# Performance work log

Hardware: AMD Instinct MI355X
Metric: run time of the kernel (lower is better)

Reference implementation:

```python
import jax, jax.numpy as jnp
import numpy as np
from jax import lax

B, S, M, D, H, T = 8, 128, 128, 256, 256, 256  # M == S required by reshape_adj; D == H required by tag FFNs and edge h0


def setup_inputs() -> dict:
    key = jax.random.key(0)
    ks = jax.random.split(key, 26)
    w = lambda k, shape: (jax.random.normal(k, shape, jnp.float32) * 0.05)
    lengths = jax.random.randint(ks[0], (B,), S // 2, S + 1)
    mask = (jnp.arange(S)[None, :] < lengths[:, None]).astype(jnp.int32)
    return {
        "input": jax.random.normal(ks[1], (B, S, D), jnp.float32),
        "tag_embeddings": jax.random.normal(ks[2], (B, S, 128), jnp.float32),
        "mask": mask,
        "head_indices": jax.random.randint(ks[3], (B, S), 0, S),
        "head_tags": jax.random.randint(ks[4], (B, S), 0, 40),
        # graph_rnn (2-layer tanh RNN, input D -> hidden H)
        "gW_ih0": w(ks[5], (H, D)), "gW_hh0": w(ks[6], (H, H)),
        "gb_ih0": w(ks[7], (H,)), "gb_hh0": w(ks[8], (H,)),
        "gW_ih1": w(ks[9], (H, H)), "gW_hh1": w(ks[10], (H, H)),
        "gb_ih1": w(ks[11], (H,)), "gb_hh1": w(ks[12], (H,)),
        # edge_rnn (2-layer tanh RNN, input M -> hidden H)
        "eW_ih0": w(ks[13], (H, M)), "eW_hh0": w(ks[14], (H, H)),
        "eb_ih0": w(ks[15], (H,)), "eb_hh0": w(ks[16], (H,)),
        "eW_ih1": w(ks[17], (H, H)), "eW_hh1": w(ks[18], (H, H)),
        "eb_ih1": w(ks[19], (H,)), "eb_hh1": w(ks[20], (H,)),
        # edge classifier + tag feedforwards
        "cls_W": w(ks[21], (1, H)), "cls_b": w(ks[22], (1,)),
        "head_W": w(ks[23], (T, H)), "head_b": jnp.zeros((T,), jnp.float32),
        "dep_W": w(ks[24], (T, H)), "dep_b": jnp.zeros((T,), jnp.float32),
    }


def _forward(input, gW_ih0, gW_hh0, gb_ih0, gb_hh0, gW_ih1, gW_hh1, gb_ih1, gb_hh1,
             eW_ih0, eW_hh0, eb_ih0, eb_hh0, eW_ih1, eW_hh1, eb_ih1, eb_hh1,
             cls_W, cls_b, head_W, head_b, dep_W, dep_b, mask):
    Bv, Sv, Dv = input.shape
    lengths = mask.sum(axis=-1)                      # [B]
    valid = jnp.arange(Sv)[:, None] < lengths[None, :]  # [S,B] packed-sequence validity

    # ---- graph_pass: 2-layer tanh RNN over time, emulating pack/pad (frozen state + zero output on pads)
    xt = input.transpose(1, 0, 2)  # [S,B,D]

    def gstep(h, inp):
        x_t, v = inp
        v = v[:, None]
        h0 = jnp.tanh(x_t @ gW_ih0.T + gb_ih0 + h[0] @ gW_hh0.T + gb_hh0)
        h0 = jnp.where(v, h0, h[0])
        h1 = jnp.tanh(h0 @ gW_ih1.T + gb_ih1 + h[1] @ gW_hh1.T + gb_hh1)
        h1 = jnp.where(v, h1, h[1])
        y = jnp.where(v, h1, 0.0)
        return jnp.stack([h0, h1]), y

    hg0 = jnp.zeros((2, Bv, H), input.dtype)
    _, ys = lax.scan(gstep, hg0, (xt, valid))
    graph_states = ys.transpose(1, 0, 2)  # [B,S,H]

    # ---- edge_pass: sequential over M steps; positions i are independent -> fold S into batch
    gs = graph_states.reshape(Bv * Sv, H)
    hE0 = jnp.stack([gs, gs])              # (edge_l=2, B*S, H)
    A0 = jnp.zeros((Bv * Sv, M), input.dtype)

    def estep(carry, j):
        A_row, h = carry
        x = A_row  # input at every step is the current (partially filled) row, per the original
        e0 = jnp.tanh(x @ eW_ih0.T + eb_ih0 + h[0] @ eW_hh0.T + eb_hh0)
        e1 = jnp.tanh(e0 @ eW_ih1.T + eb_ih1 + h[1] @ eW_hh1.T + eb_hh1)
        edge = jax.nn.sigmoid(e1 @ cls_W.T + cls_b)[:, 0]  # [B*S]
        A_row = A_row.at[:, j].set(edge)
        return (A_row, jnp.stack([e0, e1])), None

    (A_flat, _), _ = lax.scan(estep, (A0, hE0), jnp.arange(M))
    A = A_flat.reshape(Bv, Sv, M)

    # ---- reshape_adj: with M == S, shift is always 0 -> strictly-lower-triangular mask, then transpose
    tri = jnp.tril(jnp.ones((Sv, M), bool), -1)
    arc_logits = jnp.where(tri[None, :, :], A, 0.0).transpose(0, 2, 1)

    # ---- tag feedforwards (dropout = identity in eval mode)
    head_tag = jax.nn.elu(graph_states @ head_W.T + head_b)
    dep_tag = jax.nn.elu(graph_states @ dep_W.T + dep_b)
    return head_tag, dep_tag, arc_logits


def reference(input, tag_embeddings, mask, head_indices, head_tags,
              gW_ih0, gW_hh0, gb_ih0, gb_hh0, gW_ih1, gW_hh1, gb_ih1, gb_hh1,
              eW_ih0, eW_hh0, eb_ih0, eb_hh0, eW_ih1, eW_hh1, eb_ih1, eb_hh1,
              cls_W, cls_b, head_W, head_b, dep_W, dep_b):
    # tag_embeddings, head_indices, head_tags are passed through unchanged in the original
    return _forward(input, gW_ih0, gW_hh0, gb_ih0, gb_hh0, gW_ih1, gW_hh1, gb_ih1, gb_hh1,
                    eW_ih0, eW_hh0, eb_ih0, eb_hh0, eW_ih1, eW_hh1, eb_ih1, eb_hh1,
                    cls_W, cls_b, head_W, head_b, dep_W, dep_b, mask)
```

## Files before the change

kernel.cpp:

```cpp
#include <hip/hip_runtime.h>
#include <hip/hip_bf16.h>

#define HH 256
#define SS 128
#define BB 8
#define MM 128
#define DD 256
#define TT 256
#define GG 16
#define NW 8

#define ROWG 33
#define FBE (16 * ROWG * 8)
#define FB1 (ROWG * 8)

typedef float  f32x4  __attribute__((ext_vector_type(4)));
typedef short  bf16x8 __attribute__((ext_vector_type(8)));

__device__ __forceinline__ float bflo(unsigned int u) { return __uint_as_float(u << 16); }
__device__ __forceinline__ float bfhi(unsigned int u) { return __uint_as_float(u & 0xffff0000u); }
__device__ __forceinline__ float bfs(unsigned short s) { return __uint_as_float(((unsigned)s) << 16); }
__device__ __forceinline__ unsigned short f2bf(float x) {
    unsigned u = __float_as_uint(x);
    return (unsigned short)((u + 0x7fffu + ((u >> 16) & 1u)) >> 16);
}
__device__ __forceinline__ unsigned pk2bf(float a, float b) {
    return (unsigned)f2bf(a) | ((unsigned)f2bf(b) << 16);
}
__device__ __forceinline__ float ftanh(float x) {
    float e = __expf(2.0f * x);
    return 1.0f - 2.0f * __builtin_amdgcn_rcpf(e + 1.0f);
}
__device__ __forceinline__ float fsigm(float x) {
    return __builtin_amdgcn_rcpf(1.0f + __expf(-x));
}

__global__ void k_prep(const float* __restrict__ gW_hh0, const float* __restrict__ gW_ih1,
                       const float* __restrict__ gW_hh1, const float* __restrict__ eW_hh0,
                       const float* __restrict__ eW_ih1, const float* __restrict__ eW_hh1,
                       const float* __restrict__ head_W, const float* __restrict__ dep_W,
                       const float* __restrict__ eW_ih0,
                       unsigned short* __restrict__ pk_g0, unsigned short* __restrict__ pk_g1,
                       unsigned short* __restrict__ pk_g2, unsigned short* __restrict__ pk_e0,
                       unsigned short* __restrict__ pk_e1, unsigned short* __restrict__ pk_e2,
                       unsigned short* __restrict__ pk_h0, unsigned short* __restrict__ pk_h1,
                       unsigned short* __restrict__ eWTb) {
    int m = blockIdx.x >> 5;
    int blk = blockIdx.x & 31;
    if (m < 8) {
        const float* W = (m == 0) ? gW_hh0 : (m == 1) ? gW_ih1 : (m == 2) ? gW_hh1
                       : (m == 3) ? eW_hh0 : (m == 4) ? eW_ih1 : (m == 5) ? eW_hh1
                       : (m == 6) ? head_W : dep_W;
        unsigned short* pk = (m == 0) ? pk_g0 : (m == 1) ? pk_g1 : (m == 2) ? pk_g2
                           : (m == 3) ? pk_e0 : (m == 4) ? pk_e1 : (m == 5) ? pk_e2
                           : (m == 6) ? pk_h0 : pk_h1;
        int idx = blk * 256 + threadIdx.x;
        int f = idx >> 6, l = idx & 63;
        int ct = f >> 3, kb = f & 7, q = l >> 4, mm = l & 15;
        unsigned short out[8];
#pragma unroll
        for (int e = 0; e < 8; e++) {
            int k = kb * 32 + q * 4 + (e & 3) + ((e >> 2) << 4);
            out[e] = f2bf(W[(ct * 16 + mm) * HH + k]);
        }
        uint4 v;
        v.x = out[0] | ((unsigned)out[1] << 16);
        v.y = out[2] | ((unsigned)out[3] << 16);
        v.z = out[4] | ((unsigned)out[5] << 16);
        v.w = out[6] | ((unsigned)out[7] << 16);
        *(uint4*)(pk + idx * 8) = v;
    } else {
        int base = blk * 256 + threadIdx.x;
#pragma unroll
        for (int k = 0; k < 4; k++) {
            int idx = base + k * 8192;
            int j = idx >> 8, c = idx & 255;
            eWTb[idx] = f2bf(eW_ih0[c * MM + j]);
        }
    }
}

__global__ void k_x0(const float* __restrict__ x, const float* __restrict__ Wih0,
                     const float* __restrict__ bih0, const float* __restrict__ bhh0,
                     unsigned short* __restrict__ X0B) {
    int row = blockIdx.x;
    int i = threadIdx.x;
    const float4* xr = (const float4*)(x + row * DD);
    const float4* wr = (const float4*)(Wih0 + i * DD);
    float a0 = 0.f, a1 = 0.f, a2 = 0.f, a3 = 0.f;
#pragma unroll 8
    for (int k = 0; k < DD / 4; k++) {
        float4 xv = xr[k]; float4 wv = wr[k];
        a0 += xv.x * wv.x; a1 += xv.y * wv.y; a2 += xv.z * wv.z; a3 += xv.w * wv.w;
    }
    X0B[row * HH + i] = f2bf(a0 + a1 + a2 + a3 + bih0[i] + bhh0[i]);
}

__device__ __forceinline__ bf16x8 ldA(const unsigned short* __restrict__ pk, int ct, int kb, int lane) {
    return *(const bf16x8*)(pk + (((ct * 8 + kb) * 64 + lane) << 3));
}
__device__ __forceinline__ bf16x8 ldBf(const unsigned short* base, int row, int kb, int q) {
    return *(const bf16x8*)(base + ((row * ROWG + kb * 4 + q) << 3));
}

__global__ __launch_bounds__(512, 2) void k_graph_mfma(
    const unsigned short* __restrict__ X0B, const int* __restrict__ mask,
    const unsigned short* __restrict__ pk0,
    const unsigned short* __restrict__ pk1,
    const unsigned short* __restrict__ pk2,
    const float* __restrict__ bih1, const float* __restrict__ bhh1,
    float* __restrict__ GS) {
    __shared__ alignas(16) unsigned short xs[SS * HH];
    __shared__ alignas(16) unsigned short gs[SS * HH];
    __shared__ alignas(16) unsigned short h0b[2 * FB1];
    __shared__ alignas(16) unsigned short h1b[3 * FB1];
    __shared__ int lenS;

    int b = blockIdx.x;
    int tid = threadIdx.x;
    int wv = tid >> 6, lane = tid & 63;
    int q = lane >> 4, rr = lane & 15;
    int ct0 = 2 * wv;
    int m0 = 32 * wv + 4 * q;
    int g16off = (wv * 4 + q) << 3;

    { unsigned* p = (unsigned*)h0b; for (int i = tid; i < FB1; i += 512) p[i] = 0; }
    { unsigned* p = (unsigned*)h1b; for (int i = tid; i < 3 * FB1 / 2; i += 512) p[i] = 0; }
    {
        const uint4* s = (const uint4*)(X0B + b * SS * HH);
        uint4* d = (uint4*)xs;
        for (int i = tid; i < SS * HH / 8; i += 512) d[i] = s[i];
    }
    if (wv == 0) {
        int s = mask[b * SS + lane] + mask[b * SS + 64 + lane];
        for (int off = 32; off; off >>= 1) s += __shfl_xor(s, off);
        if (lane == 0) lenS = s;
    }
    bf16x8 a0[2][8], a1[2][8], a2[2][8];
#pragma unroll
    for (int kb = 0; kb < 8; kb++) {
        a0[0][kb] = ldA(pk0, ct0, kb, lane); a0[1][kb] = ldA(pk0, ct0 + 1, kb, lane);
        a1[0][kb] = ldA(pk1, ct0, kb, lane); a1[1][kb] = ldA(pk1, ct0 + 1, kb, lane);
        a2[0][kb] = ldA(pk2, ct0, kb, lane); a2[1][kb] = ldA(pk2, ct0 + 1, kb, lane);
    }
#pragma unroll
    for (int kb = 0; kb < 8; kb++) {
        asm volatile("" : "+v"(a0[0][kb]), "+v"(a0[1][kb]),
                          "+v"(a1[0][kb]), "+v"(a1[1][kb]),
                          "+v"(a2[0][kb]), "+v"(a2[1][kb]));
    }
    f32x4 b1A = *(const f32x4*)(bih1 + m0) + *(const f32x4*)(bhh1 + m0);
    f32x4 b1B = *(const f32x4*)(bih1 + m0 + 16) + *(const f32x4*)(bhh1 + m0 + 16);
    __syncthreads();
    int len = lenS;
    bool w0l = (rr == 0);

    {
        ushort4 xa = *(const ushort4*)(xs + m0);
        ushort4 xb = *(const ushort4*)(xs + m0 + 16);
        if (w0l) {
            uint4 nv = { pk2bf(ftanh(bfs(xa.x)), ftanh(bfs(xa.y))),
                         pk2bf(ftanh(bfs(xa.z)), ftanh(bfs(xa.w))),
                         pk2bf(ftanh(bfs(xb.x)), ftanh(bfs(xb.y))),
                         pk2bf(ftanh(bfs(xb.z)), ftanh(bfs(xb.w))) };
            *(uint4*)(h0b + g16off) = nv;
        }
    }
    __syncthreads();

    int ir = 2, iw = 0;
    for (int t = 1; t < len; t++) {
        const unsigned short* h0r = h0b + ((t - 1) & 1) * FB1;
        const unsigned short* h1r = h1b + ir * FB1;
        ushort4 xa = *(const ushort4*)(xs + t * 256 + m0);
        ushort4 xb = *(const ushort4*)(xs + t * 256 + m0 + 16);
        f32x4 accA0 = { bfs(xa.x), bfs(xa.y), bfs(xa.z), bfs(xa.w) };
        f32x4 accB0 = { bfs(xb.x), bfs(xb.y), bfs(xb.z), bfs(xb.w) };
        f32x4 accA1 = {0.f,0.f,0.f,0.f}, accB1 = {0.f,0.f,0.f,0.f};
        f32x4 pAe = b1A, pBe = b1B;
        f32x4 pAh = {0.f,0.f,0.f,0.f}, pBh = {0.f,0.f,0.f,0.f};
#pragma unroll
        for (int kb = 0; kb < 4; kb++) {
            bf16x8 h = ldBf(h0r, 0, kb, q);
            bf16x8 g = ldBf(h1r, 0, kb, q);
            accA0 = __builtin_amdgcn_mfma_f32_16x16x32_bf16(a0[0][kb], h, accA0, 0, 0, 0);
            accB0 = __builtin_amdgcn_mfma_f32_16x16x32_bf16(a0[1][kb], h, accB0, 0, 0, 0);
            pAe   = __builtin_amdgcn_mfma_f32_16x16x32_bf16(a1[0][kb], h, pAe, 0, 0, 0);
            pBe   = __builtin_amdgcn_mfma_f32_16x16x32_bf16(a1[1][kb], h, pBe, 0, 0, 0);
            pAh   = __builtin_amdgcn_mfma_f32_16x16x32_bf16(a2[0][kb], g, pAh, 0, 0, 0);
            pBh   = __builtin_amdgcn_mfma_f32_16x16x32_bf16(a2[1][kb], g, pBh, 0, 0, 0);
        }
#pragma unroll
        for (int kb = 4; kb < 8; kb++) {
            bf16x8 h = ldBf(h0r, 0, kb, q);
            bf16x8 g = ldBf(h1r, 0, kb, q);
            accA1 = __builtin_amdgcn_mfma_f32_16x16x32_bf16(a0[0][kb], h, accA1, 0, 0, 0);
            accB1 = __builtin_amdgcn_mfma_f32_16x16x32_bf16(a0[1][kb], h, accB1, 0, 0, 0);
            pAe   = __builtin_amdgcn_mfma_f32_16x16x32_bf16(a1[0][kb], h, pAe, 0, 0, 0);
            pBe   = __builtin_amdgcn_mfma_f32_16x16x32_bf16(a1[1][kb], h, pBe, 0, 0, 0);
            pAh   = __builtin_amdgcn_mfma_f32_16x16x32_bf16(a2[0][kb], g, pAh, 0, 0, 0);
            pBh   = __builtin_amdgcn_mfma_f32_16x16x32_bf16(a2[1][kb], g, pBh, 0, 0, 0);
        }
        if (w0l) {
            f32x4 accA = accA0 + accA1, accB = accB0 + accB1;
            uint4 nv0 = { pk2bf(ftanh(accA[0]), ftanh(accA[1])), pk2bf(ftanh(accA[2]), ftanh(accA[3])),
                          pk2bf(ftanh(accB[0]), ftanh(accB[1])), pk2bf(ftanh(accB[2]), ftanh(accB[3])) };
            *(uint4*)(h0b + (t & 1) * FB1 + g16off) = nv0;
            f32x4 pA = pAe + pAh, pB = pBe + pBh;
            float eA[4], eB[4];
#pragma unroll
            for (int r = 0; r < 4; r++) { eA[r] = ftanh(pA[r]); eB[r] = ftanh(pB[r]); }
            uint4 nv1 = { pk2bf(eA[0], eA[1]), pk2bf(eA[2], eA[3]),
                          pk2bf(eB[0], eB[1]), pk2bf(eB[2], eB[3]) };
            *(uint4*)(h1b + iw * FB1 + g16off) = nv1;
            ushort4 ga = { f2bf(eA[0]), f2bf(eA[1]), f2bf(eA[2]), f2bf(eA[3]) };
            ushort4 gb = { f2bf(eB[0]), f2bf(eB[1]), f2bf(eB[2]), f2bf(eB[3]) };
            *(ushort4*)(gs + (t - 1) * 256 + m0) = ga;
            *(ushort4*)(gs + (t - 1) * 256 + m0 + 16) = gb;
        }
        __syncthreads();
        ir = (ir + 1 == 3) ? 0 : ir + 1;
        iw = (iw + 1 == 3) ? 0 : iw + 1;
    }

    {
        const unsigned short* h0r = h0b + ((len - 1) & 1) * FB1;
        const unsigned short* h1r = h1b + ir * FB1;
        f32x4 pAe = b1A, pBe = b1B;
        f32x4 pAh = {0.f,0.f,0.f,0.f}, pBh = {0.f,0.f,0.f,0.f};
#pragma unroll
        for (int kb = 0; kb < 8; kb++) {
            bf16x8 h = ldBf(h0r, 0, kb, q);
            bf16x8 g = ldBf(h1r, 0, kb, q);
            pAe = __builtin_amdgcn_mfma_f32_16x16x32_bf16(a1[0][kb], h, pAe, 0, 0, 0);
            pBe = __builtin_amdgcn_mfma_f32_16x16x32_bf16(a1[1][kb], h, pBe, 0, 0, 0);
            pAh = __builtin_amdgcn_mfma_f32_16x16x32_bf16(a2[0][kb], g, pAh, 0, 0, 0);
            pBh = __builtin_amdgcn_mfma_f32_16x16x32_bf16(a2[1][kb], g, pBh, 0, 0, 0);
        }
        if (w0l) {
            f32x4 pA = pAe + pAh, pB = pBe + pBh;
            ushort4 ga = { f2bf(ftanh(pA[0])), f2bf(ftanh(pA[1])), f2bf(ftanh(pA[2])), f2bf(ftanh(pA[3])) };
            ushort4 gb = { f2bf(ftanh(pB[0])), f2bf(ftanh(pB[1])), f2bf(ftanh(pB[2])), f2bf(ftanh(pB[3])) };
            *(ushort4*)(gs + (len - 1) * 256 + m0) = ga;
            *(ushort4*)(gs + (len - 1) * 256 + m0 + 16) = gb;
        }
    }
    __syncthreads();
    {
        float* dst = GS + b * (SS * HH);
        const uint4* src = (const uint4*)gs;
        for (int i = tid; i < SS * HH / 8; i += 512) {
            int t = i >> 5;
            float4 f0 = {0.f,0.f,0.f,0.f}, f1 = {0.f,0.f,0.f,0.f};
            if (t < len) {
                uint4 v = src[i];
                f0 = float4{ bflo(v.x), bfhi(v.x), bflo(v.y), bfhi(v.y) };
                f1 = float4{ bflo(v.z), bfhi(v.z), bflo(v.w), bfhi(v.w) };
            }
            *(float4*)(dst + i * 8) = f0;
            *(float4*)(dst + i * 8 + 4) = f1;
        }
    }
}

__global__ __launch_bounds__(512, 2) void k_edge_mfma(
    const float* __restrict__ GS,
    const unsigned short* __restrict__ pk0,
    const unsigned short* __restrict__ pk1,
    const unsigned short* __restrict__ pk2,
    const unsigned short* __restrict__ pkh,
    const unsigned short* __restrict__ pkd,
    const unsigned short* __restrict__ eWTb,
    const float* __restrict__ bih0, const float* __restrict__ bhh0,
    const float* __restrict__ bih1, const float* __restrict__ bhh1,
    const float* __restrict__ clsW, const float* __restrict__ clsB,
    const float* __restrict__ headB, const float* __restrict__ depB,
    float* __restrict__ arc, float* __restrict__ headO, float* __restrict__ depO) {
    __shared__ alignas(16) unsigned short h0f[2 * FBE];
    __shared__ alignas(16) unsigned short h1f[2 * FBE];
    __shared__ alignas(16) unsigned short gsf[FBE];
    __shared__ alignas(16) unsigned short ews[MM * HH];
    __shared__ float red[NW][GG];
    __shared__ float cws[HH];
    __shared__ float b1s[HH];
    __shared__ float arcb[GG][MM + 1];

    int tid = threadIdx.x;
    int wv = tid >> 6, lane = tid & 63;
    int q = lane >> 4, rr = lane & 15;
    int m0 = 32 * wv + 4 * q;
    int goff = (rr * ROWG + wv * 4 + q) << 3;
    int r0 = blockIdx.x * GG;

    {
        const uint4* s = (const uint4*)eWTb;
        uint4* d = (uint4*)ews;
        for (int i = tid; i < MM * HH / 8; i += 512) d[i] = s[i];
    }
    {
        int r = tid >> 5, g = tid & 31;
        int kb = g >> 2, qq = g & 3;
        int lo = kb * 32 + qq * 4;
        const float* gp = GS + (r0 + r) * HH + lo;
        float4 vlo = *(const float4*)gp;
        float4 vhi = *(const float4*)(gp + 16);
        uint4 pv = { pk2bf(vlo.x, vlo.y), pk2bf(vlo.z, vlo.w),
                     pk2bf(vhi.x, vhi.y), pk2bf(vhi.z, vhi.w) };
        int off = (r * ROWG + g) << 3;
        *(uint4*)(h0f + FBE + off) = pv;
        *(uint4*)(h1f + FBE + off) = pv;
        *(uint4*)(gsf + off) = pv;
        *(uint4*)(h1f + off) = uint4{0,0,0,0};
        *(uint4*)(h0f + off) = uint4{0,0,0,0};
    }
    if (tid < HH) {
        cws[tid] = clsW[tid];
        b1s[tid] = bih1[tid] + bhh1[tid];
    }
    bf16x8 a0[2][8], a1[2][8], a2[2][8];
#pragma unroll
    for (int kb = 0; kb < 8; kb++) {
        a0[0][kb] = ldA(pk0, 2 * wv, kb, lane); a0[1][kb] = ldA(pk0, 2 * wv + 1, kb, lane);
        a1[0][kb] = ldA(pk1, 2 * wv, kb, lane); a1[1][kb] = ldA(pk1, 2 * wv + 1, kb, lane);
        a2[0][kb] = ldA(pk2, 2 * wv, kb, lane); a2[1][kb] = ldA(pk2, 2 * wv + 1, kb, lane);
    }
#pragma unroll
    for (int kb = 0; kb < 8; kb++) {
        asm volatile("" : "+v"(a0[0][kb]), "+v"(a0[1][kb]),
                          "+v"(a1[0][kb]), "+v"(a1[1][kb]),
                          "+v"(a2[0][kb]), "+v"(a2[1][kb]));
    }
    f32x4 xw0A = *(const f32x4*)(bih0 + m0) + *(const f32x4*)(bhh0 + m0);
    f32x4 xw0B = *(const f32x4*)(bih0 + m0 + 16) + *(const f32x4*)(bhh0 + m0 + 16);
    float clsb = clsB[0];
    int srow = (r0 + tid) & 127;
    __syncthreads();

    for (int j = 0; j <= MM; j++) {
        const unsigned short* h0r = h0f + ((j + 1) & 1) * FBE;
        const unsigned short* h1r = h1f + (j & 1) * FBE;
        f32x4 acc0 = xw0A, acc1 = xw0B;
        f32x4 p0e = *(const f32x4*)&b1s[m0];
        f32x4 p1e = *(const f32x4*)&b1s[m0 + 16];
        f32x4 p0h = {0.f,0.f,0.f,0.f}, p1h = {0.f,0.f,0.f,0.f};
#pragma unroll
        for (int kb = 0; kb < 8; kb++) {
            bf16x8 b0 = ldBf(h0r, rr, kb, q);
            bf16x8 b1 = ldBf(h1r, rr, kb, q);
            acc0 = __builtin_amdgcn_mfma_f32_16x16x32_bf16(a0[0][kb], b0, acc0, 0, 0, 0);
            acc1 = __builtin_amdgcn_mfma_f32_16x16x32_bf16(a0[1][kb], b0, acc1, 0, 0, 0);
            p0e  = __builtin_amdgcn_mfma_f32_16x16x32_bf16(a1[0][kb], b0, p0e, 0, 0, 0);
            p1e  = __builtin_amdgcn_mfma_f32_16x16x32_bf16(a1[1][kb], b0, p1e, 0, 0, 0);
            p0h  = __builtin_amdgcn_mfma_f32_16x16x32_bf16(a2[0][kb], b1, p0h, 0, 0, 0);
            p1h  = __builtin_amdgcn_mfma_f32_16x16x32_bf16(a2[1][kb], b1, p1h, 0, 0, 0);
        }
        if (j > 0) {
            float e1a[4], e1b[4];
#pragma unroll
            for (int r = 0; r < 4; r++) { e1a[r] = ftanh(p0e[r] + p0h[r]); e1b[r] = ftanh(p1e[r] + p1h[r]); }
            uint4 nv = { pk2bf(e1a[0], e1a[1]), pk2bf(e1a[2], e1a[3]),
                         pk2bf(e1b[0], e1b[1]), pk2bf(e1b[2], e1b[3]) };
            *(uint4*)(h1f + ((j + 1) & 1) * FBE + goff) = nv;
            f32x4 cwA = *(const f32x4*)&cws[m0];
            f32x4 cwB = *(const f32x4*)&cws[m0 + 16];
            float part = cwA[0] * e1a[0] + cwA[1] * e1a[1] + cwA[2] * e1a[2] + cwA[3] * e1a[3]
                       + cwB[0] * e1b[0] + cwB[1] * e1b[1] + cwB[2] * e1b[2] + cwB[3] * e1b[3];
            part += __shfl_xor(part, 16);
            part += __shfl_xor(part, 32);
            if (lane < 16) red[wv][lane] = part;
        }
        __syncthreads();
        if (j > 0) {
            float s = clsb;
#pragma unroll
            for (int w = 0; w < NW; w++) s += red[w][rr];
            float edge = fsigm(s);
            ushort4 ewcA = *(const ushort4*)(ews + (j - 1) * HH + m0);
            ushort4 ewcB = *(const ushort4*)(ews + (j - 1) * HH + m0 + 16);
            f32x4 ewA = { bfs(ewcA.x), bfs(ewcA.y), bfs(ewcA.z), bfs(ewcA.w) };
            f32x4 ewB = { bfs(ewcB.x), bfs(ewcB.y), bfs(ewcB.z), bfs(ewcB.w) };
            xw0A += edge * ewA;  acc0 += edge * ewA;
            xw0B += edge * ewB;  acc1 += edge * ewB;
            if (tid < GG) arcb[tid][j - 1] = ((j - 1) < srow) ? edge : 0.f;
        }
        if (j < MM) {
            uint4 nv = { pk2bf(ftanh(acc0[0]), ftanh(acc0[1])), pk2bf(ftanh(acc0[2]), ftanh(acc0[3])),
                         pk2bf(ftanh(acc1[0]), ftanh(acc1[1])), pk2bf(ftanh(acc1[2]), ftanh(acc1[3])) };
            *(uint4*)(h0f + (j & 1) * FBE + goff) = nv;
        }
        __syncthreads();
    }
    for (int i = tid; i < GG * MM; i += 512) {
        int row = i & 15, j = i >> 4;
        int sr = (r0 + row) & 127, bi = (r0 + row) >> 7;
        arc[bi * (MM * SS) + j * SS + sr] = arcb[row][j];
    }
    {
        f32x4 hA = *(const f32x4*)(headB + m0);
        f32x4 hB = *(const f32x4*)(headB + m0 + 16);
        f32x4 dA = *(const f32x4*)(depB + m0);
        f32x4 dB = *(const f32x4*)(depB + m0 + 16);
#pragma unroll
        for (int kb = 0; kb < 8; kb++) {
            bf16x8 bg = ldBf(gsf, rr, kb, q);
            hA = __builtin_amdgcn_mfma_f32_16x16x32_bf16(ldA(pkh, 2 * wv, kb, lane), bg, hA, 0, 0, 0);
            hB = __builtin_amdgcn_mfma_f32_16x16x32_bf16(ldA(pkh, 2 * wv + 1, kb, lane), bg, hB, 0, 0, 0);
            dA = __builtin_amdgcn_mfma_f32_16x16x32_bf16(ldA(pkd, 2 * wv, kb, lane), bg, dA, 0, 0, 0);
            dB = __builtin_amdgcn_mfma_f32_16x16x32_bf16(ldA(pkd, 2 * wv + 1, kb, lane), bg, dB, 0, 0, 0);
        }
        int row = r0 + rr;
        f32x4 oA, oB, eA, eB;
#pragma unroll
        for (int r = 0; r < 4; r++) {
            oA[r] = (hA[r] > 0.f) ? hA[r] : (__expf(hA[r]) - 1.0f);
            oB[r] = (hB[r] > 0.f) ? hB[r] : (__expf(hB[r]) - 1.0f);
            eA[r] = (dA[r] > 0.f) ? dA[r] : (__expf(dA[r]) - 1.0f);
            eB[r] = (dB[r] > 0.f) ? dB[r] : (__expf(dB[r]) - 1.0f);
        }
        *(f32x4*)(headO + row * TT + m0) = oA;
        *(f32x4*)(headO + row * TT + m0 + 16) = oB;
        *(f32x4*)(depO + row * TT + m0) = eA;
        *(f32x4*)(depO + row * TT + m0 + 16) = eB;
    }
}

extern "C" void kernel_launch(void* const* d_in, const int* in_sizes, int n_in,
                              void* d_out, int out_size, void* d_ws, size_t ws_size,
                              hipStream_t stream) {
    const float* input  = (const float*)d_in[0];
    const int*   mask   = (const int*)d_in[2];
    const float* gW_ih0 = (const float*)d_in[5];
    const float* gW_hh0 = (const float*)d_in[6];
    const float* gb_ih0 = (const float*)d_in[7];
    const float* gb_hh0 = (const float*)d_in[8];
    const float* gW_ih1 = (const float*)d_in[9];
    const float* gW_hh1 = (const float*)d_in[10];
    const float* gb_ih1 = (const float*)d_in[11];
    const float* gb_hh1 = (const float*)d_in[12];
    const float* eW_ih0 = (const float*)d_in[13];
    const float* eW_hh0 = (const float*)d_in[14];
    const float* eb_ih0 = (const float*)d_in[15];
    const float* eb_hh0 = (const float*)d_in[16];
    const float* eW_ih1 = (const float*)d_in[17];
    const float* eW_hh1 = (const float*)d_in[18];
    const float* eb_ih1 = (const float*)d_in[19];
    const float* eb_hh1 = (const float*)d_in[20];
    const float* cls_W  = (const float*)d_in[21];
    const float* cls_b  = (const float*)d_in[22];
    const float* head_W = (const float*)d_in[23];
    const float* head_b = (const float*)d_in[24];
    const float* dep_W  = (const float*)d_in[25];
    const float* dep_b  = (const float*)d_in[26];

    float* out      = (float*)d_out;
    float* head_out = out;
    float* dep_out  = out + 262144;
    float* arc_out  = out + 524288;

    char* ws = (char*)d_ws;
    unsigned short* X0B = (unsigned short*)ws;
    float* GS  = (float*)(ws + (1 << 20));
    unsigned short* pk_g0 = (unsigned short*)(ws + (2 << 20));
    unsigned short* pk_g1 = pk_g0 + 65536;
    unsigned short* pk_g2 = pk_g0 + 2 * 65536;
    unsigned short* pk_e0 = pk_g0 + 3 * 65536;
    unsigned short* pk_e1 = pk_g0 + 4 * 65536;
    unsigned short* pk_e2 = pk_g0 + 5 * 65536;
    unsigned short* pk_h0 = pk_g0 + 6 * 65536;
    unsigned short* pk_h1 = pk_g0 + 7 * 65536;
    unsigned short* eWTb  = pk_g0 + 8 * 65536;

    k_prep<<<288, 256, 0, stream>>>(gW_hh0, gW_ih1, gW_hh1, eW_hh0, eW_ih1, eW_hh1,
                                    head_W, dep_W, eW_ih0,
                                    pk_g0, pk_g1, pk_g2, pk_e0, pk_e1, pk_e2,
                                    pk_h0, pk_h1, eWTb);
    k_x0<<<1024, 256, 0, stream>>>(input, gW_ih0, gb_ih0, gb_hh0, X0B);
    k_graph_mfma<<<8, 512, 0, stream>>>(X0B, mask, pk_g0, pk_g1, pk_g2, gb_ih1, gb_hh1, GS);
    k_edge_mfma<<<64, 512, 0, stream>>>(GS, pk_e0, pk_e1, pk_e2, pk_h0, pk_h1, eWTb,
                                        eb_ih0, eb_hh0, eb_ih1, eb_hh1, cls_W, cls_b,
                                        head_b, dep_b, arc_out, head_out, dep_out);
}
```

Before: 487.3 us.

## Restructure edge RNN to four waves with in-step layer-1 dependency chain

```diff
diff --git a/kernel.cpp b/kernel.cpp
--- a/kernel.cpp
+++ b/kernel.cpp
@@ -9,6 +9,7 @@
 #define TT 256
 #define GG 16
 #define NW 8
+#define NWE 4
 
 #define ROWG 33
 #define FBE (16 * ROWG * 8)
@@ -263,7 +264,7 @@
     }
 }
 
-__global__ __launch_bounds__(512, 2) void k_edge_mfma(
+__global__ __launch_bounds__(256, 1) void k_edge_mfma(
     const float* __restrict__ GS,
     const unsigned short* __restrict__ pk0,
     const unsigned short* __restrict__ pk1,
@@ -280,7 +281,7 @@
     __shared__ alignas(16) unsigned short h1f[2 * FBE];
     __shared__ alignas(16) unsigned short gsf[FBE];
     __shared__ alignas(16) unsigned short ews[MM * HH];
-    __shared__ float red[NW][GG];
+    __shared__ float red[NWE][GG];
     __shared__ float cws[HH];
     __shared__ float b1s[HH];
     __shared__ float arcb[GG][MM + 1];
@@ -288,17 +289,19 @@
     int tid = threadIdx.x;
     int wv = tid >> 6, lane = tid & 63;
     int q = lane >> 4, rr = lane & 15;
-    int m0 = 32 * wv + 4 * q;
-    int goff = (rr * ROWG + wv * 4 + q) << 3;
     int r0 = blockIdx.x * GG;
+    int mb = 64 * wv + 4 * q;
+    int goffA = (rr * ROWG + 8 * wv + q) << 3;
+    int goffB = (rr * ROWG + 8 * wv + 4 + q) << 3;
 
     {
         const uint4* s = (const uint4*)eWTb;
         uint4* d = (uint4*)ews;
-        for (int i = tid; i < MM * HH / 8; i += 512) d[i] = s[i];
-    }
-    {
-        int r = tid >> 5, g = tid & 31;
+        for (int i = tid; i < MM * HH / 8; i += 256) d[i] = s[i];
+    }
+#pragma unroll
+    for (int rb = 0; rb < 16; rb += 8) {
+        int r = (tid >> 5) + rb, g = tid & 31;
         int kb = g >> 2, qq = g & 3;
         int lo = kb * 32 + qq * 4;
         const float* gp = GS + (r0 + r) * HH + lo;
@@ -307,120 +310,143 @@
         uint4 pv = { pk2bf(vlo.x, vlo.y), pk2bf(vlo.z, vlo.w),
                      pk2bf(vhi.x, vhi.y), pk2bf(vhi.z, vhi.w) };
         int off = (r * ROWG + g) << 3;
-        *(uint4*)(h0f + FBE + off) = pv;
-        *(uint4*)(h1f + FBE + off) = pv;
+        *(uint4*)(h0f + off) = pv;
+        *(uint4*)(h1f + off) = pv;
         *(uint4*)(gsf + off) = pv;
-        *(uint4*)(h1f + off) = uint4{0,0,0,0};
-        *(uint4*)(h0f + off) = uint4{0,0,0,0};
-    }
-    if (tid < HH) {
-        cws[tid] = clsW[tid];
-        b1s[tid] = bih1[tid] + bhh1[tid];
-    }
-    bf16x8 a0[2][8], a1[2][8], a2[2][8];
+    }
+    cws[tid] = clsW[tid];
+    b1s[tid] = bih1[tid] + bhh1[tid];
+    bf16x8 a0[4][8], a1[4][8], a2[4][8];
 #pragma unroll
     for (int kb = 0; kb < 8; kb++) {
-        a0[0][kb] = ldA(pk0, 2 * wv, kb, lane); a0[1][kb] = ldA(pk0, 2 * wv + 1, kb, lane);
-        a1[0][kb] = ldA(pk1, 2 * wv, kb, lane); a1[1][kb] = ldA(pk1, 2 * wv + 1, kb, lane);
-        a2[0][kb] = ldA(pk2, 2 * wv, kb, lane); a2[1][kb] = ldA(pk2, 2 * wv + 1, kb, lane);
+#pragma unroll
+        for (int c = 0; c < 4; c++) {
+            a0[c][kb] = ldA(pk0, 4 * wv + c, kb, lane);
+            a1[c][kb] = ldA(pk1, 4 * wv + c, kb, lane);
+            a2[c][kb] = ldA(pk2, 4 * wv + c, kb, lane);
+        }
     }
 #pragma unroll
     for (int kb = 0; kb < 8; kb++) {
-        asm volatile("" : "+v"(a0[0][kb]), "+v"(a0[1][kb]),
-                          "+v"(a1[0][kb]), "+v"(a1[1][kb]),
-                          "+v"(a2[0][kb]), "+v"(a2[1][kb]));
-    }
-    f32x4 xw0A = *(const f32x4*)(bih0 + m0) + *(const f32x4*)(bhh0 + m0);
-    f32x4 xw0B = *(const f32x4*)(bih0 + m0 + 16) + *(const f32x4*)(bhh0 + m0 + 16);
+        asm volatile("" : "+v"(a0[0][kb]), "+v"(a0[1][kb]), "+v"(a0[2][kb]), "+v"(a0[3][kb]),
+                          "+v"(a1[0][kb]), "+v"(a1[1][kb]), "+v"(a1[2][kb]), "+v"(a1[3][kb]),
+                          "+v"(a2[0][kb]), "+v"(a2[1][kb]), "+v"(a2[2][kb]), "+v"(a2[3][kb]));
+    }
+    f32x4 xw0[4];
+#pragma unroll
+    for (int c = 0; c < 4; c++) {
+        xw0[c] = *(const f32x4*)(bih0 + mb + 16 * c) + *(const f32x4*)(bhh0 + mb + 16 * c);
+    }
     float clsb = clsB[0];
     int srow = (r0 + tid) & 127;
     __syncthreads();
 
-    for (int j = 0; j <= MM; j++) {
-        const unsigned short* h0r = h0f + ((j + 1) & 1) * FBE;
-        const unsigned short* h1r = h1f + (j & 1) * FBE;
-        f32x4 acc0 = xw0A, acc1 = xw0B;
-        f32x4 p0e = *(const f32x4*)&b1s[m0];
-        f32x4 p1e = *(const f32x4*)&b1s[m0 + 16];
-        f32x4 p0h = {0.f,0.f,0.f,0.f}, p1h = {0.f,0.f,0.f,0.f};
+    for (int j = 0; j < MM; j++) {
+        int jr = j & 1, jw = jr ^ 1;
+        const unsigned short* rb0 = h0f + jr * FBE;
+        f32x4 acc[4];
+#pragma unroll
+        for (int c = 0; c < 4; c++) acc[c] = xw0[c];
 #pragma unroll
         for (int kb = 0; kb < 8; kb++) {
-            bf16x8 b0 = ldBf(h0r, rr, kb, q);
-            bf16x8 b1 = ldBf(h1r, rr, kb, q);
-            acc0 = __builtin_amdgcn_mfma_f32_16x16x32_bf16(a0[0][kb], b0, acc0, 0, 0, 0);
-            acc1 = __builtin_amdgcn_mfma_f32_16x16x32_bf16(a0[1][kb], b0, acc1, 0, 0, 0);
-            p0e  = __builtin_amdgcn_mfma_f32_16x16x32_bf16(a1[0][kb], b0, p0e, 0, 0, 0);
-            p1e  = __builtin_amdgcn_mfma_f32_16x16x32_bf16(a1[1][kb], b0, p1e, 0, 0, 0);
-            p0h  = __builtin_amdgcn_mfma_f32_16x16x32_bf16(a2[0][kb], b1, p0h, 0, 0, 0);
-            p1h  = __builtin_amdgcn_mfma_f32_16x16x32_bf16(a2[1][kb], b1, p1h, 0, 0, 0);
-        }
-        if (j > 0) {
-            float e1a[4], e1b[4];
-#pragma unroll
-            for (int r = 0; r < 4; r++) { e1a[r] = ftanh(p0e[r] + p0h[r]); e1b[r] = ftanh(p1e[r] + p1h[r]); }
-            uint4 nv = { pk2bf(e1a[0], e1a[1]), pk2bf(e1a[2], e1a[3]),
-                         pk2bf(e1b[0], e1b[1]), pk2bf(e1b[2], e1b[3]) };
-            *(uint4*)(h1f + ((j + 1) & 1) * FBE + goff) = nv;
-            f32x4 cwA = *(const f32x4*)&cws[m0];
-            f32x4 cwB = *(const f32x4*)&cws[m0 + 16];
-            float part = cwA[0] * e1a[0] + cwA[1] * e1a[1] + cwA[2] * e1a[2] + cwA[3] * e1a[3]
-                       + cwB[0] * e1b[0] + cwB[1] * e1b[1] + cwB[2] * e1b[2] + cwB[3] * e1b[3];
-            part += __shfl_xor(part, 16);
-            part += __shfl_xor(part, 32);
-            if (lane < 16) red[wv][lane] = part;
+            bf16x8 b0 = ldBf(rb0, rr, kb, q);
+#pragma unroll
+            for (int c = 0; c < 4; c++)
+                acc[c] = __builtin_amdgcn_mfma_f32_16x16x32_bf16(a0[c][kb], b0, acc[c], 0, 0, 0);
+        }
+        {
+            uint4 nvA = { pk2bf(ftanh(acc[0][0]), ftanh(acc[0][1])), pk2bf(ftanh(acc[0][2]), ftanh(acc[0][3])),
+                          pk2bf(ftanh(acc[1][0]), ftanh(acc[1][1])), pk2bf(ftanh(acc[1][2]), ftanh(acc[1][3])) };
+            uint4 nvB = { pk2bf(ftanh(acc[2][0]), ftanh(acc[2][1])), pk2bf(ftanh(acc[2][2]), ftanh(acc[2][3])),
+                          pk2bf(ftanh(acc[3][0]), ftanh(acc[3][1])), pk2bf(ftanh(acc[3][2]), ftanh(acc[3][3])) };
+            *(uint4*)(h0f + jw * FBE + goffA) = nvA;
+            *(uint4*)(h0f + jw * FBE + goffB) = nvB;
         }
         __syncthreads();
-        if (j > 0) {
-            float s = clsb;
-#pragma unroll
-            for (int w = 0; w < NW; w++) s += red[w][rr];
-            float edge = fsigm(s);
-            ushort4 ewcA = *(const ushort4*)(ews + (j - 1) * HH + m0);
-            ushort4 ewcB = *(const ushort4*)(ews + (j - 1) * HH + m0 + 16);
-            f32x4 ewA = { bfs(ewcA.x), bfs(ewcA.y), bfs(ewcA.z), bfs(ewcA.w) };
-            f32x4 ewB = { bfs(ewcB.x), bfs(ewcB.y), bfs(ewcB.z), bfs(ewcB.w) };
-            xw0A += edge * ewA;  acc0 += edge * ewA;
-            xw0B += edge * ewB;  acc1 += edge * ewB;
-            if (tid < GG) arcb[tid][j - 1] = ((j - 1) < srow) ? edge : 0.f;
-        }
-        if (j < MM) {
-            uint4 nv = { pk2bf(ftanh(acc0[0]), ftanh(acc0[1])), pk2bf(ftanh(acc0[2]), ftanh(acc0[3])),
-                         pk2bf(ftanh(acc1[0]), ftanh(acc1[1])), pk2bf(ftanh(acc1[2]), ftanh(acc1[3])) };
-            *(uint4*)(h0f + (j & 1) * FBE + goff) = nv;
-        }
+        const unsigned short* rn = h0f + jw * FBE;
+        const unsigned short* r1 = h1f + jr * FBE;
+        f32x4 p[4];
+#pragma unroll
+        for (int c = 0; c < 4; c++) p[c] = *(const f32x4*)&b1s[mb + 16 * c];
+#pragma unroll
+        for (int kb = 0; kb < 8; kb++) {
+            bf16x8 be = ldBf(rn, rr, kb, q);
+            bf16x8 bh = ldBf(r1, rr, kb, q);
+#pragma unroll
+            for (int c = 0; c < 4; c++) {
+                p[c] = __builtin_amdgcn_mfma_f32_16x16x32_bf16(a1[c][kb], be, p[c], 0, 0, 0);
+                p[c] = __builtin_amdgcn_mfma_f32_16x16x32_bf16(a2[c][kb], bh, p[c], 0, 0, 0);
+            }
+        }
+        float e1[4][4];
+        float part = 0.f;
+#pragma unroll
+        for (int c = 0; c < 4; c++) {
+            f32x4 cw = *(const f32x4*)&cws[mb + 16 * c];
+#pragma unroll
+            for (int r = 0; r < 4; r++) {
+                e1[c][r] = ftanh(p[c][r]);
+                part += cw[r] * e1[c][r];
+            }
+        }
+        {
+            uint4 nvA = { pk2bf(e1[0][0], e1[0][1]), pk2bf(e1[0][2], e1[0][3]),
+                          pk2bf(e1[1][0], e1[1][1]), pk2bf(e1[1][2], e1[1][3]) };
+            uint4 nvB = { pk2bf(e1[2][0], e1[2][1]), pk2bf(e1[2][2], e1[2][3]),
+                          pk2bf(e1[3][0], e1[3][1]), pk2bf(e1[3][2], e1[3][3]) };
+            *(uint4*)(h1f + jw * FBE + goffA) = nvA;
+            *(uint4*)(h1f + jw * FBE + goffB) = nvB;
+        }
+        part += __shfl_xor(part, 16);
+        part += __shfl_xor(part, 32);
+        if (lane < 16) red[wv][lane] = part;
         __syncthreads();
-    }
-    for (int i = tid; i < GG * MM; i += 512) {
+        float s = clsb;
+#pragma unroll
+        for (int w = 0; w < NWE; w++) s += red[w][rr];
+        float edge = fsigm(s);
+#pragma unroll
+        for (int c = 0; c < 4; c++) {
+            ushort4 ew = *(const ushort4*)(ews + j * HH + mb + 16 * c);
+            f32x4 ewf = { bfs(ew.x), bfs(ew.y), bfs(ew.z), bfs(ew.w) };
+            xw0[c] += edge * ewf;
+        }
+        if (tid < GG) arcb[tid][j] = (j < srow) ? edge : 0.f;
+    }
+    __syncthreads();
+    for (int i = tid; i < GG * MM; i += 256) {
         int row = i & 15, j = i >> 4;
         int sr = (r0 + row) & 127, bi = (r0 + row) >> 7;
         arc[bi * (MM * SS) + j * SS + sr] = arcb[row][j];
     }
     {
-        f32x4 hA = *(const f32x4*)(headB + m0);
-        f32x4 hB = *(const f32x4*)(headB + m0 + 16);
-        f32x4 dA = *(const f32x4*)(depB + m0);
-        f32x4 dB = *(const f32x4*)(depB + m0 + 16);
+        f32x4 hc[4], dc[4];
+#pragma unroll
+        for (int c = 0; c < 4; c++) {
+            hc[c] = *(const f32x4*)(headB + mb + 16 * c);
+            dc[c] = *(const f32x4*)(depB + mb + 16 * c);
+        }
 #pragma unroll
         for (int kb = 0; kb < 8; kb++) {
             bf16x8 bg = ldBf(gsf, rr, kb, q);
-            hA = __builtin_amdgcn_mfma_f32_16x16x32_bf16(ldA(pkh, 2 * wv, kb, lane), bg, hA, 0, 0, 0);
-            hB = __builtin_amdgcn_mfma_f32_16x16x32_bf16(ldA(pkh, 2 * wv + 1, kb, lane), bg, hB, 0, 0, 0);
-            dA = __builtin_amdgcn_mfma_f32_16x16x32_bf16(ldA(pkd, 2 * wv, kb, lane), bg, dA, 0, 0, 0);
-            dB = __builtin_amdgcn_mfma_f32_16x16x32_bf16(ldA(pkd, 2 * wv + 1, kb, lane), bg, dB, 0, 0, 0);
+#pragma unroll
+            for (int c = 0; c < 4; c++) {
+                hc[c] = __builtin_amdgcn_mfma_f32_16x16x32_bf16(ldA(pkh, 4 * wv + c, kb, lane), bg, hc[c], 0, 0, 0);
+                dc[c] = __builtin_amdgcn_mfma_f32_16x16x32_bf16(ldA(pkd, 4 * wv + c, kb, lane), bg, dc[c], 0, 0, 0);
+            }
         }
         int row = r0 + rr;
-        f32x4 oA, oB, eA, eB;
-#pragma unroll
-        for (int r = 0; r < 4; r++) {
-            oA[r] = (hA[r] > 0.f) ? hA[r] : (__expf(hA[r]) - 1.0f);
-            oB[r] = (hB[r] > 0.f) ? hB[r] : (__expf(hB[r]) - 1.0f);
-            eA[r] = (dA[r] > 0.f) ? dA[r] : (__expf(dA[r]) - 1.0f);
-            eB[r] = (dB[r] > 0.f) ? dB[r] : (__expf(dB[r]) - 1.0f);
-        }
-        *(f32x4*)(headO + row * TT + m0) = oA;
-        *(f32x4*)(headO + row * TT + m0 + 16) = oB;
-        *(f32x4*)(depO + row * TT + m0) = eA;
-        *(f32x4*)(depO + row * TT + m0 + 16) = eB;
+#pragma unroll
+        for (int c = 0; c < 4; c++) {
+            f32x4 ho, dd;
+#pragma unroll
+            for (int r = 0; r < 4; r++) {
+                ho[r] = (hc[c][r] > 0.f) ? hc[c][r] : (__expf(hc[c][r]) - 1.0f);
+                dd[r] = (dc[c][r] > 0.f) ? dc[c][r] : (__expf(dc[c][r]) - 1.0f);
+            }
+            *(f32x4*)(headO + row * TT + mb + 16 * c) = ho;
+            *(f32x4*)(depO + row * TT + mb + 16 * c) = dd;
+        }
     }
 }
 
@@ -476,7 +502,7 @@
                                     pk_h0, pk_h1, eWTb);
     k_x0<<<1024, 256, 0, stream>>>(input, gW_ih0, gb_ih0, gb_hh0, X0B);
     k_graph_mfma<<<8, 512, 0, stream>>>(X0B, mask, pk_g0, pk_g1, pk_g2, gb_ih1, gb_hh1, GS);
-    k_edge_mfma<<<64, 512, 0, stream>>>(GS, pk_e0, pk_e1, pk_e2, pk_h0, pk_h1, eWTb,
+    k_edge_mfma<<<64, 256, 0, stream>>>(GS, pk_e0, pk_e1, pk_e2, pk_h0, pk_h1, eWTb,
                                         eb_ih0, eb_hh0, eb_ih1, eb_hh1, cls_W, cls_b,
                                         head_b, dep_b, arc_out, head_out, dep_out);
 }
```

After: 588.6 us. +20.8%, slower.

## Unskew edge RNN loop so each step runs layer 0 then layer 1

Applied to the files above, without the earlier changes.

```diff
diff --git a/kernel.cpp b/kernel.cpp
--- a/kernel.cpp
+++ b/kernel.cpp
@@ -276,8 +276,8 @@
     const float* __restrict__ clsW, const float* __restrict__ clsB,
     const float* __restrict__ headB, const float* __restrict__ depB,
     float* __restrict__ arc, float* __restrict__ headO, float* __restrict__ depO) {
-    __shared__ alignas(16) unsigned short h0f[2 * FBE];
-    __shared__ alignas(16) unsigned short h1f[2 * FBE];
+    __shared__ alignas(16) unsigned short h0[2 * FBE];
+    __shared__ alignas(16) unsigned short h1[2 * FBE];
     __shared__ alignas(16) unsigned short gsf[FBE];
     __shared__ alignas(16) unsigned short ews[MM * HH];
     __shared__ float red[NW][GG];
@@ -307,11 +307,9 @@
         uint4 pv = { pk2bf(vlo.x, vlo.y), pk2bf(vlo.z, vlo.w),
                      pk2bf(vhi.x, vhi.y), pk2bf(vhi.z, vhi.w) };
         int off = (r * ROWG + g) << 3;
-        *(uint4*)(h0f + FBE + off) = pv;
-        *(uint4*)(h1f + FBE + off) = pv;
+        *(uint4*)(h0 + off) = pv;
+        *(uint4*)(h1 + off) = pv;
         *(uint4*)(gsf + off) = pv;
-        *(uint4*)(h1f + off) = uint4{0,0,0,0};
-        *(uint4*)(h0f + off) = uint4{0,0,0,0};
     }
     if (tid < HH) {
         cws[tid] = clsW[tid];
@@ -336,60 +334,70 @@
     int srow = (r0 + tid) & 127;
     __syncthreads();
 
-    for (int j = 0; j <= MM; j++) {
-        const unsigned short* h0r = h0f + ((j + 1) & 1) * FBE;
-        const unsigned short* h1r = h1f + (j & 1) * FBE;
+    ushort4 ewcA = *(const ushort4*)(ews + m0);
+    ushort4 ewcB = *(const ushort4*)(ews + m0 + 16);
+
+    for (int j = 0; j < MM; j++) {
+        int jr = j & 1, jw = jr ^ 1;
+        const unsigned short* rb0 = h0 + jr * FBE;
         f32x4 acc0 = xw0A, acc1 = xw0B;
+#pragma unroll
+        for (int kb = 0; kb < 8; kb++) {
+            bf16x8 b = ldBf(rb0, rr, kb, q);
+            acc0 = __builtin_amdgcn_mfma_f32_16x16x32_bf16(a0[0][kb], b, acc0, 0, 0, 0);
+            acc1 = __builtin_amdgcn_mfma_f32_16x16x32_bf16(a0[1][kb], b, acc1, 0, 0, 0);
+        }
+        {
+            uint4 nv = { pk2bf(ftanh(acc0[0]), ftanh(acc0[1])), pk2bf(ftanh(acc0[2]), ftanh(acc0[3])),
+                         pk2bf(ftanh(acc1[0]), ftanh(acc1[1])), pk2bf(ftanh(acc1[2]), ftanh(acc1[3])) };
+            *(uint4*)(h0 + jw * FBE + goff) = nv;
+        }
+        __syncthreads();
+        int jn = (j + 1 < MM) ? j + 1 : j;
+        ushort4 ewnA = *(const ushort4*)(ews + jn * HH + m0);
+        ushort4 ewnB = *(const ushort4*)(ews + jn * HH + m0 + 16);
+        const unsigned short* rn = h0 + jw * FBE;
+        const unsigned short* r1 = h1 + jr * FBE;
         f32x4 p0e = *(const f32x4*)&b1s[m0];
         f32x4 p1e = *(const f32x4*)&b1s[m0 + 16];
         f32x4 p0h = {0.f,0.f,0.f,0.f}, p1h = {0.f,0.f,0.f,0.f};
 #pragma unroll
         for (int kb = 0; kb < 8; kb++) {
-            bf16x8 b0 = ldBf(h0r, rr, kb, q);
-            bf16x8 b1 = ldBf(h1r, rr, kb, q);
-            acc0 = __builtin_amdgcn_mfma_f32_16x16x32_bf16(a0[0][kb], b0, acc0, 0, 0, 0);
-            acc1 = __builtin_amdgcn_mfma_f32_16x16x32_bf16(a0[1][kb], b0, acc1, 0, 0, 0);
-            p0e  = __builtin_amdgcn_mfma_f32_16x16x32_bf16(a1[0][kb], b0, p0e, 0, 0, 0);
-            p1e  = __builtin_amdgcn_mfma_f32_16x16x32_bf16(a1[1][kb], b0, p1e, 0, 0, 0);
-            p0h  = __builtin_amdgcn_mfma_f32_16x16x32_bf16(a2[0][kb], b1, p0h, 0, 0, 0);
-            p1h  = __builtin_amdgcn_mfma_f32_16x16x32_bf16(a2[1][kb], b1, p1h, 0, 0, 0);
-        }
-        if (j > 0) {
-            float e1a[4], e1b[4];
-#pragma unroll
-            for (int r = 0; r < 4; r++) { e1a[r] = ftanh(p0e[r] + p0h[r]); e1b[r] = ftanh(p1e[r] + p1h[r]); }
+            bf16x8 be = ldBf(rn, rr, kb, q);
+            bf16x8 bh = ldBf(r1, rr, kb, q);
+            p0e = __builtin_amdgcn_mfma_f32_16x16x32_bf16(a1[0][kb], be, p0e, 0, 0, 0);
+            p1e = __builtin_amdgcn_mfma_f32_16x16x32_bf16(a1[1][kb], be, p1e, 0, 0, 0);
+            p0h = __builtin_amdgcn_mfma_f32_16x16x32_bf16(a2[0][kb], bh, p0h, 0, 0, 0);
+            p1h = __builtin_amdgcn_mfma_f32_16x16x32_bf16(a2[1][kb], bh, p1h, 0, 0, 0);
+        }
+        float e1a[4], e1b[4];
+#pragma unroll
+        for (int r = 0; r < 4; r++) { e1a[r] = ftanh(p0e[r] + p0h[r]); e1b[r] = ftanh(p1e[r] + p1h[r]); }
+        {
             uint4 nv = { pk2bf(e1a[0], e1a[1]), pk2bf(e1a[2], e1a[3]),
                          pk2bf(e1b[0], e1b[1]), pk2bf(e1b[2], e1b[3]) };
-            *(uint4*)(h1f + ((j + 1) & 1) * FBE + goff) = nv;
-            f32x4 cwA = *(const f32x4*)&cws[m0];
-            f32x4 cwB = *(const f32x4*)&cws[m0 + 16];
-            float part = cwA[0] * e1a[0] + cwA[1] * e1a[1] + cwA[2] * e1a[2] + cwA[3] * e1a[3]
-                       + cwB[0] * e1b[0] + cwB[1] * e1b[1] + cwB[2] * e1b[2] + cwB[3] * e1b[3];
-            part += __shfl_xor(part, 16);
-            part += __shfl_xor(part, 32);
-            if (lane < 16) red[wv][lane] = part;
-        }
+            *(uint4*)(h1 + jw * FBE + goff) = nv;
+        }
+        f32x4 cwA = *(const f32x4*)&cws[m0];
+        f32x4 cwB = *(const f32x4*)&cws[m0 + 16];
+        float part = cwA[0] * e1a[0] + cwA[1] * e1a[1] + cwA[2] * e1a[2] + cwA[3] * e1a[3]
+                   + cwB[0] * e1b[0] + cwB[1] * e1b[1] + cwB[2] * e1b[2] + cwB[3] * e1b[3];
+        part += __shfl_xor(part, 16);
+        part += __shfl_xor(part, 32);
+        if (lane < 16) red[wv][lane] = part;
         __syncthreads();
-        if (j > 0) {
-            float s = clsb;
-#pragma unroll
-            for (int w = 0; w < NW; w++) s += red[w][rr];
-            float edge = fsigm(s);
-            ushort4 ewcA = *(const ushort4*)(ews + (j - 1) * HH + m0);
-            ushort4 ewcB = *(const ushort4*)(ews + (j - 1) * HH + m0 + 16);
-            f32x4 ewA = { bfs(ewcA.x), bfs(ewcA.y), bfs(ewcA.z), bfs(ewcA.w) };
-            f32x4 ewB = { bfs(ewcB.x), bfs(ewcB.y), bfs(ewcB.z), bfs(ewcB.w) };
-            xw0A += edge * ewA;  acc0 += edge * ewA;
-            xw0B += edge * ewB;  acc1 += edge * ewB;
-            if (tid < GG) arcb[tid][j - 1] = ((j - 1) < srow) ? edge : 0.f;
-        }
-        if (j < MM) {
-            uint4 nv = { pk2bf(ftanh(acc0[0]), ftanh(acc0[1])), pk2bf(ftanh(acc0[2]), ftanh(acc0[3])),
-                         pk2bf(ftanh(acc1[0]), ftanh(acc1[1])), pk2bf(ftanh(acc1[2]), ftanh(acc1[3])) };
-            *(uint4*)(h0f + (j & 1) * FBE + goff) = nv;
-        }
-        __syncthreads();
-    }
+        float s = clsb;
+#pragma unroll
+        for (int w = 0; w < NW; w++) s += red[w][rr];
+        float edge = fsigm(s);
+        f32x4 ewA = { bfs(ewcA.x), bfs(ewcA.y), bfs(ewcA.z), bfs(ewcA.w) };
+        f32x4 ewB = { bfs(ewcB.x), bfs(ewcB.y), bfs(ewcB.z), bfs(ewcB.w) };
+        xw0A += edge * ewA;
+        xw0B += edge * ewB;
+        if (tid < GG) arcb[tid][j] = (j < srow) ? edge : 0.f;
+        ewcA = ewnA; ewcB = ewnB;
+    }
+    __syncthreads();
     for (int i = tid; i < GG * MM; i += 512) {
         int row = i & 15, j = i >> 4;
         int sr = (r0 + row) & 127, bi = (r0 + row) >> 7;
```

New measurement: 505.0 us. 1.04x slower.
